# Optimization experiments

Hardware: AMD Instinct MI355X
Metric: run time of the kernel (lower is better)

The kernel has to match this reference:

```python
import jax, jax.numpy as jnp
import numpy as np

C = 32          # channel multiplicity (uvu)
SQRT3 = float(np.sqrt(3.0))
SQRT2 = float(np.sqrt(2.0))


def setup_inputs() -> dict:
    key = jax.random.key(0)
    k1, k2, k3, k4, k5 = jax.random.split(key, 5)
    V, E = 50000, 800000
    X = jax.random.normal(k1, (V, 4 * C), dtype=jnp.float32)      # 32x0e + 32x1e
    Y = jax.random.normal(k2, (E, 4), dtype=jnp.float32)          # 0e + 1e edge harmonics
    W = jax.random.normal(k3, (E, 5 * C), dtype=jnp.float32)      # per-edge weights, 5 CG paths x C
    rows = jax.random.randint(k4, (E,), 0, V, dtype=jnp.int64)    # receiver node i
    cols = jax.random.randint(k5, (E,), 0, V, dtype=jnp.int64)    # sender node j
    return {"X": X, "Y": Y, "W": W, "rows": rows, "cols": cols}


def reference(X, Y, W, rows, cols):
    V = X.shape[0]
    E = Y.shape[0]
    # split node features into scalar (l=0) and vector (l=1) channels
    x0 = X[:, :C]                       # [V, C]
    x1 = X[:, C:].reshape(V, C, 3)      # [V, C, 3]
    # gather sender features per edge
    xj0 = x0[cols]                      # [E, C]
    xj1 = x1[cols]                      # [E, C, 3]
    y0 = Y[:, 0]                        # [E]
    y1 = Y[:, 1:4]                      # [E, 3]
    w = W.reshape(E, 5, C)
    # CG paths (channelwise 'uvu'):
    # 0e x 0e -> 0e
    p00 = w[:, 0] * xj0 * y0[:, None]                                   # [E, C]
    # 0e x 1e -> 1e
    p01 = (w[:, 1] * xj0)[:, :, None] * y1[:, None, :]                  # [E, C, 3]
    # 1e x 0e -> 1e
    p10 = (w[:, 2] * y0[:, None])[:, :, None] * xj1                    # [E, C, 3]
    # 1e x 1e -> 0e  (normalized dot product)
    p110 = w[:, 3] * jnp.einsum('eck,ek->ec', xj1, y1) / SQRT3          # [E, C]
    # 1e x 1e -> 1e  (normalized cross product)
    cross = jnp.cross(xj1, y1[:, None, :])                              # [E, C, 3]
    p111 = w[:, 4][:, :, None] * cross / SQRT2                          # [E, C, 3]
    out_e = jnp.concatenate([
        p00,
        p01.reshape(E, 3 * C),
        p10.reshape(E, 3 * C),
        p110,
        p111.reshape(E, 3 * C),
    ], axis=1)                                                          # [E, 11*C]
    # scatter-add messages into receiver nodes
    Z = jax.ops.segment_sum(out_e, rows, num_segments=V)                # [V, 11*C]
    return Z
```

## Files before the change

### kernel.cpp

```cpp
#include <hip/hip_runtime.h>
#include <hip/hip_bf16.h>


#define C 32
#define ZCOLS (11 * C)
#define MAXDEG 64
#define OVF_MAX 65536
#define INV_SQRT3 0.57735026918962576451f
#define INV_SQRT2 0.70710678118654752440f

struct alignas(8) EdgeCol { int e; int c; };

__global__ void hist_scatter(const int* __restrict__ rows,
                             const int* __restrict__ cols,
                             int* __restrict__ cnt,
                             EdgeCol* __restrict__ bucket,
                             int* __restrict__ ovf_cnt,
                             int* __restrict__ ovf_list,
                             int E) {
    int e = blockIdx.x * blockDim.x + threadIdx.x;
    if (e >= E) return;
    int r = rows[e];
    int k = atomicAdd(&cnt[r], 1);
    if (k < MAXDEG) {
        EdgeCol p;
        p.e = e;
        p.c = cols[e];
        bucket[(size_t)r * MAXDEG + k] = p;
    } else {
        int o = atomicAdd(ovf_cnt, 1);
        if (o < OVF_MAX) ovf_list[o] = e;
    }
}

__global__ void tpconv_rows(const float* __restrict__ X,
                            const float* __restrict__ Y,
                            const float* __restrict__ W,
                            const int* __restrict__ cnt,
                            const EdgeCol* __restrict__ bucket,
                            float* __restrict__ Z,
                            int V) {
    const int nwaves = (gridDim.x * blockDim.x) >> 6;
    const int wave   = (blockIdx.x * blockDim.x + threadIdx.x) >> 6;
    const int lane   = threadIdx.x & 63;
    const int c = lane & 31;
    const int h = lane >> 5;

    if (wave >= V) return;

    int n_cur = cnt[wave];
    EdgeCol p_cur = bucket[(size_t)wave * MAXDEG + lane];

    for (int row = wave; row < V; row += nwaves) {
        const int row_nxt = row + nwaves;
        int n_nxt = 0;
        EdgeCol p_nxt;
        p_nxt.e = 0; p_nxt.c = 0;
        if (row_nxt < V) {
            n_nxt = cnt[row_nxt];
            p_nxt = bucket[(size_t)row_nxt * MAXDEG + lane];
        }

        int n = n_cur;
        if (n > MAXDEG) n = MAXDEG;
        int eb = p_cur.e;
        int cb = p_cur.c;

        float acc[11];
#pragma unroll
        for (int j = 0; j < 11; ++j) acc[j] = 0.0f;

        auto body = [&](int e, int col) {
            const float4 y = *reinterpret_cast<const float4*>(Y + (size_t)e * 4);

            const float* Xe = X + (size_t)col * (4 * C);
            const float xj0 = Xe[c];
            const float a0  = Xe[C + 3 * c + 0];
            const float a1  = Xe[C + 3 * c + 1];
            const float a2  = Xe[C + 3 * c + 2];

            const float* We = W + (size_t)e * (5 * C);
            const float w0 = We[0 * C + c];
            const float w1 = We[1 * C + c];
            const float w2 = We[2 * C + c];
            const float w3 = We[3 * C + c];
            const float w4 = We[4 * C + c];

            acc[0] += w0 * xj0 * y.x;

            const float t01 = w1 * xj0;
            acc[1] += t01 * y.y;
            acc[2] += t01 * y.z;
            acc[3] += t01 * y.w;

            const float t10 = w2 * y.x;
            acc[4] += t10 * a0;
            acc[5] += t10 * a1;
            acc[6] += t10 * a2;

            acc[7] += w3 * (a0 * y.y + a1 * y.z + a2 * y.w) * INV_SQRT3;

            const float s = w4 * INV_SQRT2;
            acc[8]  += s * (a1 * y.w - a2 * y.z);
            acc[9]  += s * (a2 * y.y - a0 * y.w);
            acc[10] += s * (a0 * y.z - a1 * y.y);
        };

        const int jmax = (n + 3) >> 2;
        for (int j = 0; j < jmax; ++j) {
            const int ia = 4 * j + h;
            const int ib = ia + 2;
            const int ea = __shfl(eb, ia), ca = __shfl(cb, ia);
            const int e2 = __shfl(eb, ib), c2 = __shfl(cb, ib);
            if (ia < n) body(ea, ca);
            if (ib < n) body(e2, c2);
        }

#pragma unroll
        for (int j = 0; j < 11; ++j) acc[j] += __shfl_xor(acc[j], 32);

        if (h == 0) {
            float* Zr = Z + (size_t)row * ZCOLS;
            Zr[c]                 = acc[0];
            Zr[C + 3 * c + 0]     = acc[1];
            Zr[C + 3 * c + 1]     = acc[2];
            Zr[C + 3 * c + 2]     = acc[3];
            Zr[4 * C + 3 * c + 0] = acc[4];
            Zr[4 * C + 3 * c + 1] = acc[5];
            Zr[4 * C + 3 * c + 2] = acc[6];
            Zr[7 * C + c]         = acc[7];
            Zr[8 * C + 3 * c + 0] = acc[8];
            Zr[8 * C + 3 * c + 1] = acc[9];
            Zr[8 * C + 3 * c + 2] = acc[10];
        }

        n_cur = n_nxt;
        p_cur = p_nxt;
    }
}

__global__ void ovf_apply(const float* __restrict__ X,
                          const float* __restrict__ Y,
                          const float* __restrict__ W,
                          const int* __restrict__ rows,
                          const int* __restrict__ cols,
                          const int* __restrict__ ovf_cnt,
                          const int* __restrict__ ovf_list,
                          float* __restrict__ Z) {
    int no = *ovf_cnt;
    if (no > OVF_MAX) no = OVF_MAX;
    int total = no * C;
    for (int t = blockIdx.x * blockDim.x + threadIdx.x; t < total;
         t += gridDim.x * blockDim.x) {
        const int i = t >> 5, c = t & 31;
        const int e = ovf_list[i];
        const float4 y = *reinterpret_cast<const float4*>(Y + (size_t)e * 4);
        const int row = rows[e];
        const int col = cols[e];
        const float* Xe = X + (size_t)col * (4 * C);
        const float xj0 = Xe[c];
        const float a0  = Xe[C + 3 * c + 0];
        const float a1  = Xe[C + 3 * c + 1];
        const float a2  = Xe[C + 3 * c + 2];
        const float* We = W + (size_t)e * (5 * C);
        const float w0 = We[c], w1 = We[C + c], w2 = We[2 * C + c],
                    w3 = We[3 * C + c], w4 = We[4 * C + c];
        float* Zr = Z + (size_t)row * ZCOLS;
        atomicAdd(&Zr[c], w0 * xj0 * y.x);
        const float t01 = w1 * xj0;
        atomicAdd(&Zr[C + 3 * c + 0], t01 * y.y);
        atomicAdd(&Zr[C + 3 * c + 1], t01 * y.z);
        atomicAdd(&Zr[C + 3 * c + 2], t01 * y.w);
        const float t10 = w2 * y.x;
        atomicAdd(&Zr[4 * C + 3 * c + 0], t10 * a0);
        atomicAdd(&Zr[4 * C + 3 * c + 1], t10 * a1);
        atomicAdd(&Zr[4 * C + 3 * c + 2], t10 * a2);
        atomicAdd(&Zr[7 * C + c], w3 * (a0 * y.y + a1 * y.z + a2 * y.w) * INV_SQRT3);
        const float s = w4 * INV_SQRT2;
        atomicAdd(&Zr[8 * C + 3 * c + 0], s * (a1 * y.w - a2 * y.z));
        atomicAdd(&Zr[8 * C + 3 * c + 1], s * (a2 * y.y - a0 * y.w));
        atomicAdd(&Zr[8 * C + 3 * c + 2], s * (a0 * y.z - a1 * y.y));
    }
}

extern "C" void kernel_launch(void* const* d_in, const int* in_sizes, int n_in,
                              void* d_out, int out_size, void* d_ws, size_t ws_size,
                              hipStream_t stream) {
    const float* X    = (const float*)d_in[0];
    const float* Y    = (const float*)d_in[1];
    const float* W    = (const float*)d_in[2];
    const int*   rows = (const int*)d_in[3];
    const int*   cols = (const int*)d_in[4];
    float*       Z    = (float*)d_out;

    const int E = in_sizes[1] / 4;
    const int V = in_sizes[0] / (4 * C);

    EdgeCol* bucket   = (EdgeCol*)d_ws;
    int*     cnt      = (int*)(bucket + (size_t)V * MAXDEG);
    int*     ovf_cnt  = cnt + V;
    int*     ovf_list = ovf_cnt + 1;

    hipMemsetAsync(cnt, 0, (size_t)(V + 1) * sizeof(int), stream);

    {
        const int threads = 256;
        const int blocks = (E + threads - 1) / threads;
        hist_scatter<<<blocks, threads, 0, stream>>>(rows, cols, cnt, bucket,
                                                     ovf_cnt, ovf_list, E);
    }
    {
        const int threads = 256;
        const int blocks = 1536;
        tpconv_rows<<<blocks, threads, 0, stream>>>(X, Y, W, cnt, bucket, Z, V);
    }
    {
        ovf_apply<<<64, 256, 0, stream>>>(X, Y, W, rows, cols, ovf_cnt, ovf_list, Z);
    }
}
```

Baseline: 224.0 us.

## Fuse histogram, row compute and overflow into one cooperative kernel

Merges the memset, bucket scatter, per-row tensor-product accumulation and overflow atomic pass into a single cooperative kernel separated by grid-wide syncs. Bucket capacity drops from 64 to 32 edges per row, shrinking workspace and bucket reads. Rows are now given to waves in contiguous chunks rather than strided. The aim is to remove launch gaps and the memset, at the cost of grid.sync overhead, lower parallelism sized by occupancy, and more edges spilling to the slower atomic overflow path.

```diff
diff --git a/kernel.cpp b/kernel.cpp
--- a/kernel.cpp
+++ b/kernel.cpp
@@ -1,185 +1,189 @@
 #include <hip/hip_runtime.h>
-#include <hip/hip_bf16.h>
+#include <hip/hip_cooperative_groups.h>
+
+namespace cg = cooperative_groups;
 
 
 #define C 32
 #define ZCOLS (11 * C)
-#define MAXDEG 64
+#define MAXDEG 32
 #define OVF_MAX 65536
 #define INV_SQRT3 0.57735026918962576451f
 #define INV_SQRT2 0.70710678118654752440f
 
 struct alignas(8) EdgeCol { int e; int c; };
 
-__global__ void hist_scatter(const int* __restrict__ rows,
-                             const int* __restrict__ cols,
-                             int* __restrict__ cnt,
-                             EdgeCol* __restrict__ bucket,
-                             int* __restrict__ ovf_cnt,
-                             int* __restrict__ ovf_list,
-                             int E) {
-    int e = blockIdx.x * blockDim.x + threadIdx.x;
-    if (e >= E) return;
-    int r = rows[e];
-    int k = atomicAdd(&cnt[r], 1);
-    if (k < MAXDEG) {
-        EdgeCol p;
-        p.e = e;
-        p.c = cols[e];
-        bucket[(size_t)r * MAXDEG + k] = p;
-    } else {
-        int o = atomicAdd(ovf_cnt, 1);
-        if (o < OVF_MAX) ovf_list[o] = e;
+__global__ void __launch_bounds__(256, 4)
+tpconv_fused(const float* __restrict__ X,
+             const float* __restrict__ Y,
+             const float* __restrict__ W,
+             const int* __restrict__ rows,
+             const int* __restrict__ cols,
+             float* __restrict__ Z,
+             int* __restrict__ cnt,
+             EdgeCol* __restrict__ bucket,
+             int* __restrict__ ovf_list,
+             int V, int E) {
+    cg::grid_group grid = cg::this_grid();
+    const int tid = blockIdx.x * blockDim.x + threadIdx.x;
+    const int nth = gridDim.x * blockDim.x;
+
+    for (int i = tid; i < V + 1; i += nth) cnt[i] = 0;
+    grid.sync();
+
+    int* ovf_cnt = cnt + V;
+    for (int e = tid; e < E; e += nth) {
+        const int r = rows[e];
+        const int k = atomicAdd(&cnt[r], 1);
+        if (k < MAXDEG) {
+            EdgeCol p; p.e = e; p.c = cols[e];
+            bucket[(size_t)r * MAXDEG + k] = p;
+        } else {
+            const int o = atomicAdd(ovf_cnt, 1);
+            if (o < OVF_MAX) ovf_list[o] = e;
+        }
     }
-}
-
-__global__ void tpconv_rows(const float* __restrict__ X,
-                            const float* __restrict__ Y,
-                            const float* __restrict__ W,
-                            const int* __restrict__ cnt,
-                            const EdgeCol* __restrict__ bucket,
-                            float* __restrict__ Z,
-                            int V) {
-    const int nwaves = (gridDim.x * blockDim.x) >> 6;
-    const int wave   = (blockIdx.x * blockDim.x + threadIdx.x) >> 6;
-    const int lane   = threadIdx.x & 63;
-    const int c = lane & 31;
-    const int h = lane >> 5;
-
-    if (wave >= V) return;
-
-    int n_cur = cnt[wave];
-    EdgeCol p_cur = bucket[(size_t)wave * MAXDEG + lane];
-
-    for (int row = wave; row < V; row += nwaves) {
-        const int row_nxt = row + nwaves;
-        int n_nxt = 0;
-        EdgeCol p_nxt;
-        p_nxt.e = 0; p_nxt.c = 0;
-        if (row_nxt < V) {
-            n_nxt = cnt[row_nxt];
-            p_nxt = bucket[(size_t)row_nxt * MAXDEG + lane];
+    __threadfence();
+    grid.sync();
+
+    {
+        const int nwaves = nth >> 6;
+        const int wave   = tid >> 6;
+        const int lane   = threadIdx.x & 63;
+        const int c = lane & 31;
+        const int h = lane >> 5;
+        const int rpw = (V + nwaves - 1) / nwaves;
+        const int r0 = wave * rpw;
+        const int r1 = (r0 + rpw < V) ? (r0 + rpw) : V;
+
+        if (r0 < V) {
+            int n_cur = cnt[r0];
+            EdgeCol p_cur; p_cur.e = 0; p_cur.c = 0;
+            if (lane < MAXDEG) p_cur = bucket[(size_t)r0 * MAXDEG + lane];
+
+            for (int row = r0; row < r1; ++row) {
+                int n_nxt = 0;
+                EdgeCol p_nxt; p_nxt.e = 0; p_nxt.c = 0;
+                if (row + 1 < r1) {
+                    n_nxt = cnt[row + 1];
+                    if (lane < MAXDEG) p_nxt = bucket[(size_t)(row + 1) * MAXDEG + lane];
+                }
+
+                int n = n_cur;
+                if (n > MAXDEG) n = MAXDEG;
+                const int eb = p_cur.e;
+                const int cb = p_cur.c;
+
+                float acc[11];
+#pragma unroll
+                for (int j = 0; j < 11; ++j) acc[j] = 0.0f;
+
+                auto body = [&](int e, int col) {
+                    const float4 y = *reinterpret_cast<const float4*>(Y + (size_t)e * 4);
+
+                    const float* Xe = X + (size_t)col * (4 * C);
+                    const float xj0 = Xe[c];
+                    const float a0  = Xe[C + 3 * c + 0];
+                    const float a1  = Xe[C + 3 * c + 1];
+                    const float a2  = Xe[C + 3 * c + 2];
+
+                    const float* We = W + (size_t)e * (5 * C);
+                    const float w0 = We[0 * C + c];
+                    const float w1 = We[1 * C + c];
+                    const float w2 = We[2 * C + c];
+                    const float w3 = We[3 * C + c];
+                    const float w4 = We[4 * C + c];
+
+                    acc[0] += w0 * xj0 * y.x;
+
+                    const float t01 = w1 * xj0;
+                    acc[1] += t01 * y.y;
+                    acc[2] += t01 * y.z;
+                    acc[3] += t01 * y.w;
+
+                    const float t10 = w2 * y.x;
+                    acc[4] += t10 * a0;
+                    acc[5] += t10 * a1;
+                    acc[6] += t10 * a2;
+
+                    acc[7] += w3 * (a0 * y.y + a1 * y.z + a2 * y.w) * INV_SQRT3;
+
+                    const float s = w4 * INV_SQRT2;
+                    acc[8]  += s * (a1 * y.w - a2 * y.z);
+                    acc[9]  += s * (a2 * y.y - a0 * y.w);
+                    acc[10] += s * (a0 * y.z - a1 * y.y);
+                };
+
+                const int jmax = (n + 3) >> 2;
+                for (int j = 0; j < jmax; ++j) {
+                    const int ia = 4 * j + h;
+                    const int ib = ia + 2;
+                    const int ea = __shfl(eb, ia), ca = __shfl(cb, ia);
+                    const int e2 = __shfl(eb, ib), c2 = __shfl(cb, ib);
+                    if (ia < n) body(ea, ca);
+                    if (ib < n) body(e2, c2);
+                }
+
+#pragma unroll
+                for (int j = 0; j < 11; ++j) acc[j] += __shfl_xor(acc[j], 32);
+
+                if (h == 0) {
+                    float* Zr = Z + (size_t)row * ZCOLS;
+                    Zr[c]                 = acc[0];
+                    Zr[C + 3 * c + 0]     = acc[1];
+                    Zr[C + 3 * c + 1]     = acc[2];
+                    Zr[C + 3 * c + 2]     = acc[3];
+                    Zr[4 * C + 3 * c + 0] = acc[4];
+                    Zr[4 * C + 3 * c + 1] = acc[5];
+                    Zr[4 * C + 3 * c + 2] = acc[6];
+                    Zr[7 * C + c]         = acc[7];
+                    Zr[8 * C + 3 * c + 0] = acc[8];
+                    Zr[8 * C + 3 * c + 1] = acc[9];
+                    Zr[8 * C + 3 * c + 2] = acc[10];
+                }
+
+                n_cur = n_nxt;
+                p_cur = p_nxt;
+            }
         }
-
-        int n = n_cur;
-        if (n > MAXDEG) n = MAXDEG;
-        int eb = p_cur.e;
-        int cb = p_cur.c;
-
-        float acc[11];
-#pragma unroll
-        for (int j = 0; j < 11; ++j) acc[j] = 0.0f;
-
-        auto body = [&](int e, int col) {
+    }
+    __threadfence();
+    grid.sync();
+
+    {
+        int no = *ovf_cnt;
+        if (no > OVF_MAX) no = OVF_MAX;
+        const int total = no * C;
+        for (int t = tid; t < total; t += nth) {
+            const int i = t >> 5, c = t & 31;
+            const int e = ovf_list[i];
             const float4 y = *reinterpret_cast<const float4*>(Y + (size_t)e * 4);
-
+            const int row = rows[e];
+            const int col = cols[e];
             const float* Xe = X + (size_t)col * (4 * C);
             const float xj0 = Xe[c];
             const float a0  = Xe[C + 3 * c + 0];
             const float a1  = Xe[C + 3 * c + 1];
             const float a2  = Xe[C + 3 * c + 2];
-
             const float* We = W + (size_t)e * (5 * C);
-            const float w0 = We[0 * C + c];
-            const float w1 = We[1 * C + c];
-            const float w2 = We[2 * C + c];
-            const float w3 = We[3 * C + c];
-            const float w4 = We[4 * C + c];
-
-            acc[0] += w0 * xj0 * y.x;
-
+            const float w0 = We[c], w1 = We[C + c], w2 = We[2 * C + c],
+                        w3 = We[3 * C + c], w4 = We[4 * C + c];
+            float* Zr = Z + (size_t)row * ZCOLS;
+            atomicAdd(&Zr[c], w0 * xj0 * y.x);
             const float t01 = w1 * xj0;
-            acc[1] += t01 * y.y;
-            acc[2] += t01 * y.z;
-            acc[3] += t01 * y.w;
-
+            atomicAdd(&Zr[C + 3 * c + 0], t01 * y.y);
+            atomicAdd(&Zr[C + 3 * c + 1], t01 * y.z);
+            atomicAdd(&Zr[C + 3 * c + 2], t01 * y.w);
             const float t10 = w2 * y.x;
-            acc[4] += t10 * a0;
-            acc[5] += t10 * a1;
-            acc[6] += t10 * a2;
-
-            acc[7] += w3 * (a0 * y.y + a1 * y.z + a2 * y.w) * INV_SQRT3;
-
+            atomicAdd(&Zr[4 * C + 3 * c + 0], t10 * a0);
+            atomicAdd(&Zr[4 * C + 3 * c + 1], t10 * a1);
+            atomicAdd(&Zr[4 * C + 3 * c + 2], t10 * a2);
+            atomicAdd(&Zr[7 * C + c], w3 * (a0 * y.y + a1 * y.z + a2 * y.w) * INV_SQRT3);
             const float s = w4 * INV_SQRT2;
-            acc[8]  += s * (a1 * y.w - a2 * y.z);
-            acc[9]  += s * (a2 * y.y - a0 * y.w);
-            acc[10] += s * (a0 * y.z - a1 * y.y);
-        };
-
-        const int jmax = (n + 3) >> 2;
-        for (int j = 0; j < jmax; ++j) {
-            const int ia = 4 * j + h;
-            const int ib = ia + 2;
-            const int ea = __shfl(eb, ia), ca = __shfl(cb, ia);
-            const int e2 = __shfl(eb, ib), c2 = __shfl(cb, ib);
-            if (ia < n) body(ea, ca);
-            if (ib < n) body(e2, c2);
+            atomicAdd(&Zr[8 * C + 3 * c + 0], s * (a1 * y.w - a2 * y.z));
+            atomicAdd(&Zr[8 * C + 3 * c + 1], s * (a2 * y.y - a0 * y.w));
+            atomicAdd(&Zr[8 * C + 3 * c + 2], s * (a0 * y.z - a1 * y.y));
         }
-
-#pragma unroll
-        for (int j = 0; j < 11; ++j) acc[j] += __shfl_xor(acc[j], 32);
-
-        if (h == 0) {
-            float* Zr = Z + (size_t)row * ZCOLS;
-            Zr[c]                 = acc[0];
-            Zr[C + 3 * c + 0]     = acc[1];
-            Zr[C + 3 * c + 1]     = acc[2];
-            Zr[C + 3 * c + 2]     = acc[3];
-            Zr[4 * C + 3 * c + 0] = acc[4];
-            Zr[4 * C + 3 * c + 1] = acc[5];
-            Zr[4 * C + 3 * c + 2] = acc[6];
-            Zr[7 * C + c]         = acc[7];
-            Zr[8 * C + 3 * c + 0] = acc[8];
-            Zr[8 * C + 3 * c + 1] = acc[9];
-            Zr[8 * C + 3 * c + 2] = acc[10];
-        }
-
-        n_cur = n_nxt;
-        p_cur = p_nxt;
-    }
-}
-
-__global__ void ovf_apply(const float* __restrict__ X,
-                          const float* __restrict__ Y,
-                          const float* __restrict__ W,
-                          const int* __restrict__ rows,
-                          const int* __restrict__ cols,
-                          const int* __restrict__ ovf_cnt,
-                          const int* __restrict__ ovf_list,
-                          float* __restrict__ Z) {
-    int no = *ovf_cnt;
-    if (no > OVF_MAX) no = OVF_MAX;
-    int total = no * C;
-    for (int t = blockIdx.x * blockDim.x + threadIdx.x; t < total;
-         t += gridDim.x * blockDim.x) {
-        const int i = t >> 5, c = t & 31;
-        const int e = ovf_list[i];
-        const float4 y = *reinterpret_cast<const float4*>(Y + (size_t)e * 4);
-        const int row = rows[e];
-        const int col = cols[e];
-        const float* Xe = X + (size_t)col * (4 * C);
-        const float xj0 = Xe[c];
-        const float a0  = Xe[C + 3 * c + 0];
-        const float a1  = Xe[C + 3 * c + 1];
-        const float a2  = Xe[C + 3 * c + 2];
-        const float* We = W + (size_t)e * (5 * C);
-        const float w0 = We[c], w1 = We[C + c], w2 = We[2 * C + c],
-                    w3 = We[3 * C + c], w4 = We[4 * C + c];
-        float* Zr = Z + (size_t)row * ZCOLS;
-        atomicAdd(&Zr[c], w0 * xj0 * y.x);
-        const float t01 = w1 * xj0;
-        atomicAdd(&Zr[C + 3 * c + 0], t01 * y.y);
-        atomicAdd(&Zr[C + 3 * c + 1], t01 * y.z);
-        atomicAdd(&Zr[C + 3 * c + 2], t01 * y.w);
-        const float t10 = w2 * y.x;
-        atomicAdd(&Zr[4 * C + 3 * c + 0], t10 * a0);
-        atomicAdd(&Zr[4 * C + 3 * c + 1], t10 * a1);
-        atomicAdd(&Zr[4 * C + 3 * c + 2], t10 * a2);
-        atomicAdd(&Zr[7 * C + c], w3 * (a0 * y.y + a1 * y.z + a2 * y.w) * INV_SQRT3);
-        const float s = w4 * INV_SQRT2;
-        atomicAdd(&Zr[8 * C + 3 * c + 0], s * (a1 * y.w - a2 * y.z));
-        atomicAdd(&Zr[8 * C + 3 * c + 1], s * (a2 * y.y - a0 * y.w));
-        atomicAdd(&Zr[8 * C + 3 * c + 2], s * (a0 * y.z - a1 * y.y));
     }
 }
 
@@ -193,28 +197,27 @@
     const int*   cols = (const int*)d_in[4];
     float*       Z    = (float*)d_out;
 
-    const int E = in_sizes[1] / 4;
-    const int V = in_sizes[0] / (4 * C);
+    int E = in_sizes[1] / 4;
+    int V = in_sizes[0] / (4 * C);
 
     EdgeCol* bucket   = (EdgeCol*)d_ws;
     int*     cnt      = (int*)(bucket + (size_t)V * MAXDEG);
-    int*     ovf_cnt  = cnt + V;
-    int*     ovf_list = ovf_cnt + 1;
-
-    hipMemsetAsync(cnt, 0, (size_t)(V + 1) * sizeof(int), stream);
-
-    {
-        const int threads = 256;
-        const int blocks = (E + threads - 1) / threads;
-        hist_scatter<<<blocks, threads, 0, stream>>>(rows, cols, cnt, bucket,
-                                                     ovf_cnt, ovf_list, E);
-    }
-    {
-        const int threads = 256;
-        const int blocks = 1536;
-        tpconv_rows<<<blocks, threads, 0, stream>>>(X, Y, W, cnt, bucket, Z, V);
-    }
-    {
-        ovf_apply<<<64, 256, 0, stream>>>(X, Y, W, rows, cols, ovf_cnt, ovf_list, Z);
-    }
+    int*     ovf_list = cnt + (V + 1);
+
+    int perCU = 0;
+    hipError_t oerr = hipOccupancyMaxActiveBlocksPerMultiprocessor(
+        &perCU, (const void*)tpconv_fused, 256, 0);
+    if (oerr != hipSuccess || perCU < 1) perCU = 2;
+    if (perCU > 8) perCU = 8;
+    int numCU = 256;
+    hipDeviceProp_t props;
+    if (hipGetDeviceProperties(&props, 0) == hipSuccess && props.multiProcessorCount > 0)
+        numCU = props.multiProcessorCount;
+    int nblocks = perCU * numCU;
+
+    void* args[] = {(void*)&X, (void*)&Y, (void*)&W, (void*)&rows, (void*)&cols,
+                    (void*)&Z, (void*)&cnt, (void*)&bucket, (void*)&ovf_list,
+                    (void*)&V, (void*)&E};
+    hipLaunchCooperativeKernel((const void*)tpconv_fused,
+                               dim3(nblocks), dim3(256), args, 0, stream);
 }
```

Result: slower. 772.3 us (+244.7%).

## Shrink edge buckets to int ids, cap degree at 32, load cols in consumer

Applied to the files above, without the earlier changes.

Each bucket entry now stores only the edge id instead of an (edge, col) pair, and the per-row capacity drops from 64 to 32 slots. The sender index is read from cols inside the row-processing kernel instead of in the histogram kernel, and the row kernel's grid grows from 1536 to 2048 blocks. The aim is to cut workspace writes and reads in the bucketing pass and to raise occupancy. In exchange, each edge costs an extra dependent cols load, and rows with more than 32 edges (mean degree is 16) now spill more entries to the slower atomic overflow path.

```diff
diff --git a/kernel.cpp b/kernel.cpp
--- a/kernel.cpp
+++ b/kernel.cpp
@@ -4,17 +4,14 @@
 
 #define C 32
 #define ZCOLS (11 * C)
-#define MAXDEG 64
+#define MAXDEG 32
 #define OVF_MAX 65536
 #define INV_SQRT3 0.57735026918962576451f
 #define INV_SQRT2 0.70710678118654752440f
 
-struct alignas(8) EdgeCol { int e; int c; };
-
 __global__ void hist_scatter(const int* __restrict__ rows,
-                             const int* __restrict__ cols,
                              int* __restrict__ cnt,
-                             EdgeCol* __restrict__ bucket,
+                             int* __restrict__ bucket,
                              int* __restrict__ ovf_cnt,
                              int* __restrict__ ovf_list,
                              int E) {
@@ -23,10 +20,7 @@
     int r = rows[e];
     int k = atomicAdd(&cnt[r], 1);
     if (k < MAXDEG) {
-        EdgeCol p;
-        p.e = e;
-        p.c = cols[e];
-        bucket[(size_t)r * MAXDEG + k] = p;
+        bucket[(size_t)r * MAXDEG + k] = e;
     } else {
         int o = atomicAdd(ovf_cnt, 1);
         if (o < OVF_MAX) ovf_list[o] = e;
@@ -36,8 +30,9 @@
 __global__ void tpconv_rows(const float* __restrict__ X,
                             const float* __restrict__ Y,
                             const float* __restrict__ W,
+                            const int* __restrict__ cols,
                             const int* __restrict__ cnt,
-                            const EdgeCol* __restrict__ bucket,
+                            const int* __restrict__ bucket,
                             float* __restrict__ Z,
                             int V) {
     const int nwaves = (gridDim.x * blockDim.x) >> 6;
@@ -49,29 +44,28 @@
     if (wave >= V) return;
 
     int n_cur = cnt[wave];
-    EdgeCol p_cur = bucket[(size_t)wave * MAXDEG + lane];
+    int e_cur = (lane < MAXDEG) ? bucket[(size_t)wave * MAXDEG + lane] : 0;
 
     for (int row = wave; row < V; row += nwaves) {
         const int row_nxt = row + nwaves;
         int n_nxt = 0;
-        EdgeCol p_nxt;
-        p_nxt.e = 0; p_nxt.c = 0;
+        int e_nxt = 0;
         if (row_nxt < V) {
             n_nxt = cnt[row_nxt];
-            p_nxt = bucket[(size_t)row_nxt * MAXDEG + lane];
+            if (lane < MAXDEG) e_nxt = bucket[(size_t)row_nxt * MAXDEG + lane];
         }
 
         int n = n_cur;
         if (n > MAXDEG) n = MAXDEG;
-        int eb = p_cur.e;
-        int cb = p_cur.c;
+        const int eb = e_cur;
 
         float acc[11];
 #pragma unroll
         for (int j = 0; j < 11; ++j) acc[j] = 0.0f;
 
-        auto body = [&](int e, int col) {
+        auto body = [&](int e) {
             const float4 y = *reinterpret_cast<const float4*>(Y + (size_t)e * 4);
+            const int col = cols[e];
 
             const float* Xe = X + (size_t)col * (4 * C);
             const float xj0 = Xe[c];
@@ -110,10 +104,10 @@
         for (int j = 0; j < jmax; ++j) {
             const int ia = 4 * j + h;
             const int ib = ia + 2;
-            const int ea = __shfl(eb, ia), ca = __shfl(cb, ia);
-            const int e2 = __shfl(eb, ib), c2 = __shfl(cb, ib);
-            if (ia < n) body(ea, ca);
-            if (ib < n) body(e2, c2);
+            const int ea = __shfl(eb, ia);
+            const int e2 = __shfl(eb, ib);
+            if (ia < n) body(ea);
+            if (ib < n) body(e2);
         }
 
 #pragma unroll
@@ -135,7 +129,7 @@
         }
 
         n_cur = n_nxt;
-        p_cur = p_nxt;
+        e_cur = e_nxt;
     }
 }
 
@@ -196,23 +190,23 @@
     const int E = in_sizes[1] / 4;
     const int V = in_sizes[0] / (4 * C);
 
-    EdgeCol* bucket   = (EdgeCol*)d_ws;
-    int*     cnt      = (int*)(bucket + (size_t)V * MAXDEG);
-    int*     ovf_cnt  = cnt + V;
-    int*     ovf_list = ovf_cnt + 1;
+    int* bucket   = (int*)d_ws;
+    int* cnt      = bucket + (size_t)V * MAXDEG;
+    int* ovf_cnt  = cnt + V;
+    int* ovf_list = ovf_cnt + 1;
 
     hipMemsetAsync(cnt, 0, (size_t)(V + 1) * sizeof(int), stream);
 
     {
         const int threads = 256;
         const int blocks = (E + threads - 1) / threads;
-        hist_scatter<<<blocks, threads, 0, stream>>>(rows, cols, cnt, bucket,
-                                                     ovf_cnt, ovf_list, E);
+        hist_scatter<<<blocks, threads, 0, stream>>>(rows, cnt, bucket, ovf_cnt,
+                                                     ovf_list, E);
     }
     {
         const int threads = 256;
-        const int blocks = 1536;
-        tpconv_rows<<<blocks, threads, 0, stream>>>(X, Y, W, cnt, bucket, Z, V);
+        const int blocks = 2048;
+        tpconv_rows<<<blocks, threads, 0, stream>>>(X, Y, W, cols, cnt, bucket, Z, V);
     }
     {
         ovf_apply<<<64, 256, 0, stream>>>(X, Y, W, rows, cols, ovf_cnt, ovf_list, Z);
```

Result: slower. 234.3 us (+4.6%).
